# Optimization experiments

Hardware: AMD Instinct MI355X
Metric: run time of the kernel (lower is better)

Reference implementation:

```python
import jax, jax.numpy as jnp
import numpy as np

N = 8          # num_nodes (forced: stack with deconv output of leading dim 64 = 8*8)
T = 10         # out_dim == num_steps (Conv1d(out_dim, 1, ...) runs over the time axis)
H = 64         # hidden_dim (forced: ConvTranspose1d in_channels=64)
E = 2 * N      # edges come in fwd/rev pairs; E/2 must equal N for avg_pool squeeze
NODE_IN = 512  # gat1 in_dim = x_feat width (510) + CNN_1 output (2)
EDGE_IN = 128


def _conv1d(x, w, b, pad):
    # x: [B, Cin, L], w: [Cout, Cin, K]
    y = jax.lax.conv_general_dilated(x, w, (1,), [(pad, pad)],
                                     dimension_numbers=('NCH', 'OIH', 'NCH'))
    return y + b[None, :, None]


def _gat(x, src, dst, ea, W, a_s, a_d, We, a_e, bias, heads, ch, concat):
    # PyG GATConv with edge_dim and default add_self_loops=True (mean-fill edge_attr)
    n = x.shape[0]
    loop = jnp.arange(n)
    src = jnp.concatenate([src, loop])
    dst = jnp.concatenate([dst, loop])
    ea = jnp.concatenate([ea, jnp.broadcast_to(ea.mean(0), (n, ea.shape[1]))], 0)
    h = (x @ W).reshape(n, heads, ch)                 # [N,H,C]
    he = (ea @ We).reshape(-1, heads, ch)             # [E+N,H,C]
    alpha = (h * a_s).sum(-1)[src] + (h * a_d).sum(-1)[dst] + (he * a_e).sum(-1)
    alpha = jax.nn.leaky_relu(alpha, 0.2)             # [E+N,H]
    amax = jax.ops.segment_max(alpha, dst, num_segments=n)
    ex = jnp.exp(alpha - amax[dst])
    den = jax.ops.segment_sum(ex, dst, num_segments=n)
    w = ex / (den[dst] + 1e-16)                       # scatter-softmax over dst
    out = jax.ops.segment_sum(w[:, :, None] * h[src], dst, num_segments=n)
    out = out.reshape(n, heads * ch) if concat else out.mean(1)
    return out + bias


def _forward(x_feat, x_feat_tmp, edge_attr, c1w1, c1b1, c1w2, c1b2,
             g1_lin, g1_as, g1_ad, g1_le, g1_ae, g1_b,
             g2_lin, g2_as, g2_ad, g2_le, g2_ae, g2_b,
             mlp_w1, mlp_b1, mlp_w2, mlp_b2,
             d1w, d1b, d2w, d2b, d3w, d3b,
             c2w1, c2b1, c2w2, c2b2, c2l1w, c2l1b, c2l2w, c2l2b,
             edge_index):
    src, dst = edge_index[0], edge_index[1]
    # ---- CNN_1 on rows 1 and 5 of x_feat_tmp ----
    t = jnp.stack([x_feat_tmp[1], x_feat_tmp[5]], axis=1)    # [N,2,T]
    t = t.reshape(2, N, T)                                   # torch .view semantics
    t = jax.nn.relu(_conv1d(t, c1w1, c1b1, 1))               # [2,N,T]
    t = _conv1d(jnp.transpose(t, (0, 2, 1)), c1w2, c1b2, 1)  # [2,1,N]
    x_ = jax.nn.relu(t.reshape(N, 2))                        # torch .view semantics
    # ---- GAT stack ----
    x = jnp.concatenate([x_feat, x_], axis=1)                # [N,512]
    x = jax.nn.relu(_gat(x, src, dst, edge_attr, g1_lin, g1_as, g1_ad,
                         g1_le, g1_ae, g1_b, 4, H, True))    # [N,256]
    ea_new = jax.nn.relu(edge_attr @ mlp_w1 + mlp_b1) @ mlp_w2 + mlp_b2  # [E,64]
    x = jax.nn.relu(_gat(x, src, dst, ea_new, g2_lin, g2_as, g2_ad,
                         g2_le, g2_ae, g2_b, 1, H, False))   # [N,64]
    # ---- ConvTranspose1d on length-1 input == einsum; avg_pool2d over nodes/edges ----
    x_pool = (jnp.einsum('ni,iot->not', x, d1w) + d1b[None, :, None]).mean(0)          # [64,10]
    ef = (jnp.einsum('ni,iot->not', ea_new[::2], d2w) + d2b[None, :, None]).mean(0)    # [64,10]
    er = (jnp.einsum('ni,iot->not', ea_new[1::2], d3w) + d3b[None, :, None]).mean(0)   # [64,10]
    inf = x_feat_tmp.reshape(N * N, T)                       # [64,10]
    # ---- CNN_2 ----
    c = jnp.stack([x_pool, inf, ef, er], axis=1)             # [64,4,10]
    c = _conv1d(c, c2w1, c2b1, 0)                            # [64,32,8]
    c = c.reshape(N * N, 32, 4, 2).max(-1)                   # MaxPool1d(2) -> [64,32,4]
    c = _conv1d(c, c2w2, c2b2, 0)                            # [64,64,2]
    c = c.reshape(N * N, 128)                                # Flatten(1,2)
    c = jax.nn.relu((c @ c2l1w + c2l1b) @ c2l2w + c2l2b)     # [64,10]
    return c.reshape(N, N, T)


def setup_inputs():
    ks = iter(jax.random.split(jax.random.key(0), 48))
    def rn(shape, s=0.1):
        return jax.random.normal(next(ks), shape, dtype=jnp.float32) * s
    return dict(
        x_feat=rn((N, NODE_IN - 2), 1.0),
        x_feat_tmp=rn((N, N, T), 1.0),
        edge_attr=rn((E, EDGE_IN), 1.0),
        c1w1=rn((N, N, 3)), c1b1=rn((N,)),
        c1w2=rn((1, T, 3)), c1b2=rn((1,)),
        g1_lin=rn((NODE_IN, 4 * H)), g1_as=rn((4, H)), g1_ad=rn((4, H)),
        g1_le=rn((EDGE_IN, 4 * H)), g1_ae=rn((4, H)), g1_b=rn((4 * H,)),
        g2_lin=rn((4 * H, H)), g2_as=rn((1, H)), g2_ad=rn((1, H)),
        g2_le=rn((H, H)), g2_ae=rn((1, H)), g2_b=rn((H,)),
        mlp_w1=rn((EDGE_IN, H)), mlp_b1=rn((H,)),
        mlp_w2=rn((H, H)), mlp_b2=rn((H,)),
        d1w=rn((H, H, 10)), d1b=rn((H,)),
        d2w=rn((H, H, 10)), d2b=rn((H,)),
        d3w=rn((H, H, 10)), d3b=rn((H,)),
        c2w1=rn((32, 4, 3)), c2b1=rn((32,)),
        c2w2=rn((64, 32, 3)), c2b2=rn((64,)),
        c2l1w=rn((128, 256)), c2l1b=rn((256,)),
        c2l2w=rn((256, T)), c2l2b=rn((T,)),
        edge_index=jax.random.randint(next(ks), (2, E), 0, N, dtype=jnp.int32),
    )


def reference(x_feat, x_feat_tmp, edge_attr, c1w1, c1b1, c1w2, c1b2,
              g1_lin, g1_as, g1_ad, g1_le, g1_ae, g1_b,
              g2_lin, g2_as, g2_ad, g2_le, g2_ae, g2_b,
              mlp_w1, mlp_b1, mlp_w2, mlp_b2,
              d1w, d1b, d2w, d2b, d3w, d3b,
              c2w1, c2b1, c2w2, c2b2, c2l1w, c2l1b, c2l2w, c2l2b,
              edge_index):
    return _forward(x_feat, x_feat_tmp, edge_attr, c1w1, c1b1, c1w2, c1b2,
                    g1_lin, g1_as, g1_ad, g1_le, g1_ae, g1_b,
                    g2_lin, g2_as, g2_ad, g2_le, g2_ae, g2_b,
                    mlp_w1, mlp_b1, mlp_w2, mlp_b2,
                    d1w, d1b, d2w, d2b, d3w, d3b,
                    c2w1, c2b1, c2w2, c2b2, c2l1w, c2l1b, c2l2w, c2l2b,
                    edge_index)
```

## Files before the change

kernel.cpp:

```cpp
#include <hip/hip_runtime.h>
#include <math.h>

#define WS_HXPART 0
#define WS_SMALL  16384
#define WS_XCNN   16384
#define WS_SE1    16400
#define WS_SE2    16468
#define WS_WF     16488
#define WS_BF     17768
#define WS_VM     17778

#define F_H    0
#define F_X1   2048
#define F_H2P  4096
#define F_H2   6144
#define F_X2   6656
#define F_G1AS 7168
#define F_G1AD 7424
#define F_G1B  7680
#define F_GL0  7936
#define F_GL1  8192
#define F_G2AS 8448
#define F_G2AD 8512
#define F_G2B  8576
#define F_SS1  8704
#define F_SD1  8736
#define F_AL1  8768
#define F_WT1  8864
#define F_MX1  8960
#define F_DN1  8992
#define F_A1   9024
#define F_SS2  9280
#define F_SD2  9288
#define F_AL2  9296
#define F_WT2  9320
#define F_MX2  9344
#define F_DN2  9352
#define F_A2   9360
#define F_SA   0
#define F_SW2  7680
#define F_SML  13824
#define SM_XCNN 0
#define SM_SE1  16
#define SM_SE2  84
#define SM_WF   104
#define SM_BF   1384
#define SM_VM   1394
#define F_SW1  15424
#define F_CIN  15808
#define F_ESRC 15968
#define F_EDST 15992
#define F_SB1  16016
#define F_SB2  16048
#define F_SDB  16112

__global__ __launch_bounds__(256) void k1_pre(
    const float* __restrict__ xf,   const float* __restrict__ xft,
    const float* __restrict__ ea,
    const float* __restrict__ c1w1, const float* __restrict__ c1b1,
    const float* __restrict__ c1w2, const float* __restrict__ c1b2,
    const float* __restrict__ g1lin,const float* __restrict__ g1le,
    const float* __restrict__ g1ae,
    const float* __restrict__ mw1,  const float* __restrict__ mb1,
    const float* __restrict__ mw2,  const float* __restrict__ mb2,
    const float* __restrict__ g2le, const float* __restrict__ g2ae,
    const float* __restrict__ l1w,  const float* __restrict__ l1b,
    const float* __restrict__ l2w,  const float* __restrict__ l2b,
    float* __restrict__ ws)
{
    const int b = blockIdx.x, tid = threadIdx.x;
    if (b < 8) {
        __shared__ float sx[512];
        const int k0 = b * 64;
        const int klen = (b == 7) ? 62 : 64;
        for (int idx = tid; idx < 512; idx += 256) {
            int n = idx >> 6, kk = idx & 63;
            sx[n * 64 + kk] = (kk < klen) ? xf[n * 510 + k0 + kk] : 0.f;
        }
        __syncthreads();
        float acc[8];
        #pragma unroll
        for (int n = 0; n < 8; ++n) acc[n] = 0.f;
        for (int kk = 0; kk < 64; ++kk) {
            float w = g1lin[(k0 + kk) * 256 + tid];
            #pragma unroll
            for (int n = 0; n < 8; ++n) acc[n] += sx[n * 64 + kk] * w;
        }
        #pragma unroll
        for (int n = 0; n < 8; ++n) ws[WS_HXPART + (b * 8 + n) * 256 + tid] = acc[n];
    } else if (b == 8) {
        __shared__ float sea[2048 + 128];
        __shared__ float sae[256], q1[512];
        for (int idx = tid; idx < 2048; idx += 256) sea[idx] = ea[idx];
        sae[tid] = g1ae[tid];
        __syncthreads();
        if (tid < 128) {
            float m = 0.f;
            for (int e = 0; e < 16; ++e) m += sea[e * 128 + tid];
            sea[2048 + tid] = m * (1.f / 16.f);
        }
        __syncthreads();
        for (int o = tid; o < 512; o += 256) {
            int k = o >> 2, hd = o & 3;
            float acc = 0.f;
            for (int c = 0; c < 64; ++c) acc += g1le[k * 256 + hd * 64 + c] * sae[hd * 64 + c];
            q1[o] = acc;
        }
        __syncthreads();
        if (tid < 64) {
            int e = tid >> 2, hd = tid & 3;
            float acc = 0.f;
            for (int k = 0; k < 128; ++k) acc += sea[e * 128 + k] * q1[k * 4 + hd];
            ws[WS_SE1 + tid] = acc;
        } else if (tid < 68) {
            int hd = tid - 64;
            float acc = 0.f;
            for (int k = 0; k < 128; ++k) acc += sea[2048 + k] * q1[k * 4 + hd];
            ws[WS_SE1 + 64 + hd] = acc;
        }
    } else if (b == 9) {
        __shared__ float sea[2048];
        __shared__ float tmp[1024];
        __shared__ float ean[17 * 64];
        __shared__ float sq2a[64], sq2[64];
        for (int idx = tid; idx < 2048; idx += 256) sea[idx] = ea[idx];
        if (tid < 64) sq2a[tid] = g2ae[tid];
        __syncthreads();
        for (int o = tid; o < 1024; o += 256) {
            int e = o >> 6, c = o & 63;
            float acc = mb1[c];
            for (int k = 0; k < 128; ++k) acc += sea[e * 128 + k] * mw1[k * 64 + c];
            tmp[o] = fmaxf(acc, 0.f);
        }
        __syncthreads();
        for (int o = tid; o < 1024; o += 256) {
            int e = o >> 6, c = o & 63;
            float acc = mb2[c];
            for (int k = 0; k < 64; ++k) acc += tmp[e * 64 + k] * mw2[k * 64 + c];
            ean[o] = acc;
        }
        __syncthreads();
        if (tid < 64) {
            float m = 0.f;
            for (int e = 0; e < 16; ++e) m += ean[e * 64 + tid];
            ean[1024 + tid] = m * (1.f / 16.f);
        } else if (tid < 128) {
            int c = tid - 64;
            float m = 0.f;
            for (int e = 0; e < 16; e += 2) m += ean[e * 64 + c];
            ws[WS_VM + 64 + c] = m * 0.125f;
        } else if (tid < 192) {
            int c = tid - 128;
            float m = 0.f;
            for (int e = 1; e < 16; e += 2) m += ean[e * 64 + c];
            ws[WS_VM + 128 + c] = m * 0.125f;
        }
        __syncthreads();
        if (tid < 64) {
            float acc = 0.f;
            for (int c = 0; c < 64; ++c) acc += g2le[tid * 64 + c] * sq2a[c];
            sq2[tid] = acc;
        }
        __syncthreads();
        if (tid < 16) {
            float acc = 0.f;
            for (int k = 0; k < 64; ++k) acc += ean[tid * 64 + k] * sq2[k];
            ws[WS_SE2 + tid] = acc;
        } else if (tid == 16) {
            float acc = 0.f;
            for (int k = 0; k < 64; ++k) acc += ean[1024 + k] * sq2[k];
            ws[WS_SE2 + 16] = acc;
        }
    } else if (b == 10) {
        __shared__ float t2[160], y1[160], y2[16];
        if (tid < 160) {
            int b_ = tid / 80, ch = (tid % 80) / 10, tt = tid % 10;
            int srow = ((ch & 1) == 0) ? 1 : 5;
            int n = 4 * b_ + (ch >> 1);
            t2[tid] = xft[srow * 80 + n * 10 + tt];
        }
        __syncthreads();
        if (tid < 160) {
            int b_ = tid / 80, co = (tid % 80) / 10, tt = tid % 10;
            float acc = c1b1[co];
            for (int ci = 0; ci < 8; ++ci)
                for (int k = 0; k < 3; ++k) {
                    int p = tt + k - 1;
                    if (p >= 0 && p < 10) acc += t2[b_ * 80 + ci * 10 + p] * c1w1[co * 24 + ci * 3 + k];
                }
            y1[tid] = fmaxf(acc, 0.f);
        }
        __syncthreads();
        if (tid < 16) {
            int b_ = tid >> 3, p = tid & 7;
            float acc = c1b2[0];
            for (int i = 0; i < 10; ++i)
                for (int k = 0; k < 3; ++k) {
                    int q = p + k - 1;
                    if (q >= 0 && q < 8) acc += y1[b_ * 80 + q * 10 + i] * c1w2[i * 3 + k];
                }
            y2[tid] = acc;
        }
        __syncthreads();
        if (tid < 16) ws[WS_XCNN + tid] = fmaxf(y2[tid], 0.f);
    } else {
        __shared__ float sl2[2560];
        for (int idx = tid; idx < 2560; idx += 256) sl2[idx] = l2w[idx];
        __syncthreads();
        const int m0 = (b - 11) * 32;
        for (int o = tid; o < 320; o += 256) {
            int ml = o / 10, t = o % 10, m = m0 + ml;
            float acc = 0.f;
            for (int j = 0; j < 256; ++j) acc += l1w[m * 256 + j] * sl2[j * 10 + t];
            ws[WS_WF + m * 10 + t] = acc;
        }
        if (b == 11 && tid < 10) {
            float acc = l2b[tid];
            for (int j = 0; j < 256; ++j) acc += l1b[j] * sl2[j * 10 + tid];
            ws[WS_BF + tid] = acc;
        }
    }
}

__global__ __launch_bounds__(512) void k2_main(
    const float* __restrict__ xft,
    const float* __restrict__ g1lin,
    const float* __restrict__ g1as, const float* __restrict__ g1ad,
    const float* __restrict__ g1b,
    const float* __restrict__ g2lin,
    const float* __restrict__ g2as, const float* __restrict__ g2ad,
    const float* __restrict__ g2b,
    const int* __restrict__ eidx,
    const float* __restrict__ d1w, const float* __restrict__ d1b,
    const float* __restrict__ d2w, const float* __restrict__ d2b,
    const float* __restrict__ d3w, const float* __restrict__ d3b,
    const float* __restrict__ c2w1, const float* __restrict__ c2b1,
    const float* __restrict__ c2w2, const float* __restrict__ c2b2,
    const float* __restrict__ ws, float* __restrict__ out)
{
    __shared__ float sm[16128];
    const int tid = threadIdx.x;
    const int r0 = blockIdx.x * 4;
    int* esrc = (int*)sm + F_ESRC;
    int* edst = (int*)sm + F_EDST;

    float rA[15], rW[12];
    #pragma unroll
    for (int i = 0; i < 15; ++i) {
        int idx = tid + 512 * i;
        int t = idx % 10, rl = (idx / 10) & 3, ii = idx / 40;
        int tau = ii >> 6, iC = ii & 63;
        const float* dw = (tau == 0) ? d1w : (tau == 1) ? d2w : d3w;
        rA[i] = dw[iC * 640 + (r0 + rl) * 10 + t];
    }
    #pragma unroll
    for (int i = 0; i < 12; ++i) rW[i] = c2w2[tid + 512 * i];
    for (int idx = tid; idx < 1600; idx += 512) sm[F_SML + idx] = ws[WS_SMALL + idx];
    for (int idx = tid; idx < 384;  idx += 512) sm[F_SW1 + idx] = c2w1[idx];
    if (tid < 256) {
        sm[F_G1AS + tid] = g1as[tid];
        sm[F_G1AD + tid] = g1ad[tid];
        sm[F_G1B  + tid] = g1b[tid];
        sm[F_GL0  + tid] = g1lin[510 * 256 + tid];
        sm[F_GL1  + tid] = g1lin[511 * 256 + tid];
    } else {
        int j = tid - 256;
        if (j < 64)       { sm[F_G2AS + j] = g2as[j]; sm[F_G2AD + j] = g2ad[j]; sm[F_G2B + j] = g2b[j]; }
        else if (j < 88)  { int i = j - 64;  esrc[i] = (i < 16) ? eidx[i] : i - 16;
                                             edst[i] = (i < 16) ? eidx[16 + i] : i - 16; }
        else if (j < 128) { int i = j - 88;  int rl = i / 10, t = i % 10;
                            sm[F_CIN + rl * 40 + 10 + t] = xft[(r0 + rl) * 10 + t]; }
        else if (j < 160) sm[F_SB1 + j - 128] = c2b1[j - 128];
        else if (j < 224) sm[F_SB2 + j - 160] = c2b2[j - 160];
        else if (j < 236) { int i = j - 224, tau = i / 4, rl = i % 4;
                            const float* db = (tau == 0) ? d1b : (tau == 1) ? d2b : d3b;
                            sm[F_SDB + i] = db[r0 + rl]; }
    }
    __syncthreads();

    {
        const int j = tid & 255, half = tid >> 8;
        for (int nl = 0; nl < 4; ++nl) {
            int n = half * 4 + nl;
            float acc = 0.f;
            #pragma unroll
            for (int cb = 0; cb < 8; ++cb) acc += ws[WS_HXPART + (cb * 8 + n) * 256 + j];
            acc += sm[F_SML + SM_XCNN + n * 2] * sm[F_GL0 + j]
                 + sm[F_SML + SM_XCNN + n * 2 + 1] * sm[F_GL1 + j];
            sm[F_H + n * 256 + j] = acc;
        }
    }
    __syncthreads();
    {
        int p = tid >> 4, g = tid & 15, n = p >> 2, hd = p & 3;
        float aS = 0.f, aD = 0.f;
        #pragma unroll
        for (int cc = 0; cc < 4; ++cc) {
            int c = (((cc + p) & 3) << 4) + g;
            float hv = sm[F_H + n * 256 + hd * 64 + c];
            aS += hv * sm[F_G1AS + hd * 64 + c];
            aD += hv * sm[F_G1AD + hd * 64 + c];
        }
        #pragma unroll
        for (int m = 8; m >= 1; m >>= 1) { aS += __shfl_xor(aS, m); aD += __shfl_xor(aD, m); }
        if (g == 0) { sm[F_SS1 + p] = aS; sm[F_SD1 + p] = aD; }
    }
    __syncthreads();
    if (tid < 96) {
        int e = tid >> 2, hd = tid & 3;
        float se = (e < 16) ? sm[F_SML + SM_SE1 + tid] : sm[F_SML + SM_SE1 + 64 + hd];
        float s = sm[F_SS1 + esrc[e] * 4 + hd] + sm[F_SD1 + edst[e] * 4 + hd] + se;
        sm[F_AL1 + tid] = (s > 0.f) ? s : 0.2f * s;
    }
    __syncthreads();
    {
        int p = tid >> 4, g = tid & 15, n = p >> 2, hd = p & 3;
        float v1 = (edst[g] == n) ? sm[F_AL1 + g * 4 + hd] : -1e30f;
        float v2 = (g < 8 && edst[g + 16] == n) ? sm[F_AL1 + (g + 16) * 4 + hd] : -1e30f;
        float mx = fmaxf(v1, v2);
        #pragma unroll
        for (int m = 8; m >= 1; m >>= 1) mx = fmaxf(mx, __shfl_xor(mx, m));
        float ex = expf(v1 - mx) + ((g < 8) ? expf(v2 - mx) : 0.f);
        #pragma unroll
        for (int m = 8; m >= 1; m >>= 1) ex += __shfl_xor(ex, m);
        if (g == 0) { sm[F_MX1 + p] = mx; sm[F_DN1 + p] = ex; }
    }
    __syncthreads();
    if (tid < 96) {
        int e = tid >> 2, hd = tid & 3, d = edst[e];
        sm[F_WT1 + tid] = expf(sm[F_AL1 + tid] - sm[F_MX1 + d * 4 + hd]) / (sm[F_DN1 + d * 4 + hd] + 1e-16f);
    }
    __syncthreads();
    if (tid < 256) {
        int s = tid >> 5, n = (tid >> 2) & 7, hd = tid & 3;
        float acc = 0.f;
        #pragma unroll
        for (int e = 0; e < 24; ++e)
            acc += (edst[e] == n && esrc[e] == s) ? sm[F_WT1 + e * 4 + hd] : 0.f;
        sm[F_A1 + tid] = acc;
    }
    __syncthreads();
    {
        const int j = tid & 255, half = tid >> 8, hd = j >> 6;
        for (int nl = 0; nl < 4; ++nl) {
            int n = half * 4 + nl;
            float acc = 0.f;
            #pragma unroll
            for (int s = 0; s < 8; ++s)
                acc += sm[F_A1 + s * 32 + n * 4 + hd] * sm[F_H + s * 256 + j];
            sm[F_X1 + n * 256 + j] = fmaxf(acc + sm[F_G1B + j], 0.f);
        }
    }
    __syncthreads();
    {
        const int kc = tid >> 7, sub = (tid >> 6) & 1, c = tid & 63;
        float p0 = 0.f, p1 = 0.f, p2 = 0.f, p3 = 0.f;
        for (int kk = 0; kk < 64; ++kk) {
            int k = kc * 64 + kk;
            float g = g2lin[k * 64 + c];
            p0 += sm[F_X1 + (sub * 4 + 0) * 256 + k] * g;
            p1 += sm[F_X1 + (sub * 4 + 1) * 256 + k] * g;
            p2 += sm[F_X1 + (sub * 4 + 2) * 256 + k] * g;
            p3 += sm[F_X1 + (sub * 4 + 3) * 256 + k] * g;
        }
        sm[F_H2P + kc * 512 + (sub * 4 + 0) * 64 + c] = p0;
        sm[F_H2P + kc * 512 + (sub * 4 + 1) * 64 + c] = p1;
        sm[F_H2P + kc * 512 + (sub * 4 + 2) * 64 + c] = p2;
        sm[F_H2P + kc * 512 + (sub * 4 + 3) * 64 + c] = p3;
    }
    __syncthreads();
    sm[F_H2 + tid] = sm[F_H2P + tid] + sm[F_H2P + 512 + tid]
                   + sm[F_H2P + 1024 + tid] + sm[F_H2P + 1536 + tid];
    __syncthreads();
    {
        int n = tid >> 6, c = tid & 63;
        float hv = sm[F_H2 + n * 64 + c];
        float aS = hv * sm[F_G2AS + c], aD = hv * sm[F_G2AD + c];
        #pragma unroll
        for (int m = 32; m >= 1; m >>= 1) { aS += __shfl_xor(aS, m); aD += __shfl_xor(aD, m); }
        if (c == 0) { sm[F_SS2 + n] = aS; sm[F_SD2 + n] = aD; }
    }
    __syncthreads();
    if (tid < 24) {
        float se = (tid < 16) ? sm[F_SML + SM_SE2 + tid] : sm[F_SML + SM_SE2 + 16];
        float s = sm[F_SS2 + esrc[tid]] + sm[F_SD2 + edst[tid]] + se;
        sm[F_AL2 + tid] = (s > 0.f) ? s : 0.2f * s;
    }
    __syncthreads();
    if (tid < 256) {
        int n = tid >> 5, g = tid & 31;
        float v = (g < 24 && edst[g] == n) ? sm[F_AL2 + g] : -1e30f;
        float mx = v;
        #pragma unroll
        for (int m = 16; m >= 1; m >>= 1) mx = fmaxf(mx, __shfl_xor(mx, m));
        float ex = expf(v - mx);
        #pragma unroll
        for (int m = 16; m >= 1; m >>= 1) ex += __shfl_xor(ex, m);
        if (g == 0) { sm[F_MX2 + n] = mx; sm[F_DN2 + n] = ex; }
    }
    __syncthreads();
    if (tid < 24) {
        int d = edst[tid];
        sm[F_WT2 + tid] = expf(sm[F_AL2 + tid] - sm[F_MX2 + d]) / (sm[F_DN2 + d] + 1e-16f);
    }
    __syncthreads();
    if (tid < 64) {
        int n = tid >> 3, s = tid & 7;
        float acc = 0.f;
        #pragma unroll
        for (int e = 0; e < 24; ++e)
            acc += (edst[e] == n && esrc[e] == s) ? sm[F_WT2 + e] : 0.f;
        sm[F_A2 + tid] = acc;
    }
    __syncthreads();
    {
        int n = tid >> 6, c = tid & 63;
        float acc = 0.f;
        #pragma unroll
        for (int s = 0; s < 8; ++s) acc += sm[F_A2 + n * 8 + s] * sm[F_H2 + s * 64 + c];
        sm[F_X2 + n * 64 + c] = fmaxf(acc + sm[F_G2B + c], 0.f);
    }
    __syncthreads();
    if (tid < 64) {
        float m = 0.f;
        #pragma unroll
        for (int n = 0; n < 8; ++n) m += sm[F_X2 + n * 64 + tid];
        sm[F_SML + SM_VM + tid] = m * 0.125f;
    }
    __syncthreads();

    #pragma unroll
    for (int i = 0; i < 15; ++i) sm[F_SA + tid + 512 * i] = rA[i];
    #pragma unroll
    for (int i = 0; i < 12; ++i) sm[F_SW2 + tid + 512 * i] = rW[i];
    __syncthreads();
    if (tid < 120) {
        int t = tid % 10, tau = (tid / 10) % 3, rl = tid / 30;
        float acc = sm[F_SDB + tau * 4 + rl];
        for (int i = 0; i < 64; ++i)
            acc += sm[F_SML + SM_VM + tau * 64 + i] * sm[F_SA + ((tau * 64 + i) * 4 + rl) * 10 + t];
        int ch = (tau == 0) ? 0 : (tau + 1);
        sm[F_CIN + rl * 40 + ch * 10 + t] = acc;
    }
    __syncthreads();
    for (int o = tid; o < 1024; o += 512) {
        int rl = o >> 8, co = (o >> 3) & 31, p = o & 7;
        float acc = sm[F_SB1 + co];
        #pragma unroll
        for (int ci = 0; ci < 4; ++ci)
            #pragma unroll
            for (int k = 0; k < 3; ++k)
                acc += sm[F_CIN + rl * 40 + ci * 10 + p + k] * sm[F_SW1 + co * 12 + ci * 3 + k];
        sm[F_SA + o] = acc;
    }
    __syncthreads();
    {
        int rl = tid >> 7, co = (tid >> 2) & 31, q = tid & 3;
        sm[F_SA + 1024 + tid] = fmaxf(sm[F_SA + rl * 256 + co * 8 + 2 * q],
                                      sm[F_SA + rl * 256 + co * 8 + 2 * q + 1]);
    }
    __syncthreads();
    {
        int rl = tid >> 7, m = tid & 127, co2 = m >> 1, p = m & 1;
        float acc = sm[F_SB2 + co2];
        for (int ci = 0; ci < 32; ++ci)
            #pragma unroll
            for (int k = 0; k < 3; ++k)
                acc += sm[F_SA + 1024 + rl * 128 + ci * 4 + p + k] * sm[F_SW2 + co2 * 96 + ci * 3 + k];
        sm[F_SA + 1536 + tid] = acc;
    }
    __syncthreads();
    if (tid < 40) {
        int rl = tid / 10, t = tid % 10;
        float acc = sm[F_SML + SM_BF + t];
        for (int m = 0; m < 128; ++m)
            acc += sm[F_SA + 1536 + rl * 128 + m] * sm[F_SML + SM_WF + m * 10 + t];
        out[(r0 + rl) * 10 + t] = fmaxf(acc, 0.f);
    }
}

extern "C" void kernel_launch(void* const* d_in, const int* in_sizes, int n_in,
                              void* d_out, int out_size, void* d_ws, size_t ws_size,
                              hipStream_t stream)
{
    const float* xf    = (const float*)d_in[0];
    const float* xft   = (const float*)d_in[1];
    const float* ea    = (const float*)d_in[2];
    const float* c1w1  = (const float*)d_in[3];
    const float* c1b1  = (const float*)d_in[4];
    const float* c1w2  = (const float*)d_in[5];
    const float* c1b2  = (const float*)d_in[6];
    const float* g1lin = (const float*)d_in[7];
    const float* g1as  = (const float*)d_in[8];
    const float* g1ad  = (const float*)d_in[9];
    const float* g1le  = (const float*)d_in[10];
    const float* g1ae  = (const float*)d_in[11];
    const float* g1b   = (const float*)d_in[12];
    const float* g2lin = (const float*)d_in[13];
    const float* g2as  = (const float*)d_in[14];
    const float* g2ad  = (const float*)d_in[15];
    const float* g2le  = (const float*)d_in[16];
    const float* g2ae  = (const float*)d_in[17];
    const float* g2b   = (const float*)d_in[18];
    const float* mw1   = (const float*)d_in[19];
    const float* mb1   = (const float*)d_in[20];
    const float* mw2   = (const float*)d_in[21];
    const float* mb2   = (const float*)d_in[22];
    const float* d1w   = (const float*)d_in[23];
    const float* d1b   = (const float*)d_in[24];
    const float* d2w   = (const float*)d_in[25];
    const float* d2b   = (const float*)d_in[26];
    const float* d3w   = (const float*)d_in[27];
    const float* d3b   = (const float*)d_in[28];
    const float* c2w1  = (const float*)d_in[29];
    const float* c2b1  = (const float*)d_in[30];
    const float* c2w2  = (const float*)d_in[31];
    const float* c2b2  = (const float*)d_in[32];
    const float* l1w   = (const float*)d_in[33];
    const float* l1b   = (const float*)d_in[34];
    const float* l2w   = (const float*)d_in[35];
    const float* l2b   = (const float*)d_in[36];
    const int*   eidx  = (const int*)d_in[37];
    float* ws  = (float*)d_ws;
    float* out = (float*)d_out;

    hipLaunchKernelGGL(k1_pre, dim3(15), dim3(256), 0, stream,
        xf, xft, ea, c1w1, c1b1, c1w2, c1b2,
        g1lin, g1le, g1ae, mw1, mb1, mw2, mb2,
        g2le, g2ae, l1w, l1b, l2w, l2b, ws);
    hipLaunchKernelGGL(k2_main, dim3(16), dim3(512), 0, stream,
        xft, g1lin, g1as, g1ad, g1b,
        g2lin, g2as, g2ad, g2b, eidx,
        d1w, d1b, d2w, d2b, d3w, d3b,
        c2w1, c2b1, c2w2, c2b2, ws, out);
}
```

Measured before the change: 33.13 us.

## Restructure pre-kernel split and shorten main-kernel sync chain

The pre-kernel splits the x@W1 contraction into 4 k-chunks instead of 8 and stores the partials interleaved, so the main kernel reads them with one float4 load per node. The edge-embedding projection is split across two blocks. The main kernel prefetches those partials into registers, folds the leaky-relu alpha computations and the maxpool into their consumers to remove several barriers, and splits the deconv and final linear reductions across threads with shuffles. It also warms g2lin with dummy loads. The trade is more redundant recomputation and register pressure in exchange for fewer synchronization stages.

```diff
diff --git a/kernel.cpp b/kernel.cpp
--- a/kernel.cpp
+++ b/kernel.cpp
@@ -2,50 +2,43 @@
 #include <math.h>
 
 #define WS_HXPART 0
-#define WS_SMALL  16384
-#define WS_XCNN   16384
-#define WS_SE1    16400
-#define WS_SE2    16468
-#define WS_WF     16488
-#define WS_BF     17768
-#define WS_VM     17778
+#define WS_SMALL  8192
+#define SM_XCNN 0
+#define SM_SE1A 16
+#define SM_SE1B 84
+#define SM_SE2  152
+#define SM_WF   172
+#define SM_BF   1452
+#define SM_VME  1462
+#define SM_SIZE 1600
 
 #define F_H    0
 #define F_X1   2048
 #define F_H2P  4096
-#define F_H2   6144
-#define F_X2   6656
-#define F_G1AS 7168
-#define F_G1AD 7424
-#define F_G1B  7680
-#define F_GL0  7936
-#define F_GL1  8192
-#define F_G2AS 8448
-#define F_G2AD 8512
-#define F_G2B  8576
-#define F_SS1  8704
-#define F_SD1  8736
-#define F_AL1  8768
-#define F_WT1  8864
-#define F_MX1  8960
-#define F_DN1  8992
-#define F_A1   9024
-#define F_SS2  9280
-#define F_SD2  9288
-#define F_AL2  9296
-#define F_WT2  9320
-#define F_MX2  9344
-#define F_DN2  9352
-#define F_A2   9360
-#define F_SA   0
+#define F_GL0  6144
+#define F_GL1  6400
+#define F_G1AS 6656
+#define F_G1AD 6912
+#define F_G1B  7168
+#define F_SS1  7424
+#define F_SD1  7456
+#define F_MX1  7488
+#define F_DN1  7520
+#define F_WT1  7552
 #define F_SW2  7680
+#define F_A1   7680
+#define F_H2   7936
+#define F_X2   8448
+#define F_G2AS 8960
+#define F_G2AD 9024
+#define F_G2B  9088
+#define F_SS2  9152
+#define F_SD2  9160
+#define F_MX2  9168
+#define F_DN2  9176
+#define F_A2   9184
+#define F_WT2  9248
 #define F_SML  13824
-#define SM_XCNN 0
-#define SM_SE1  16
-#define SM_SE2  84
-#define SM_WF   104
-#define SM_BF   1384
-#define SM_VM   1394
 #define F_SW1  15424
 #define F_CIN  15808
 #define F_ESRC 15968
@@ -53,6 +46,8 @@
 #define F_SB1  16016
 #define F_SB2  16048
 #define F_SDB  16112
+#define F_VM0  16128
+#define SM_TOT 16192
 
 __global__ __launch_bounds__(256) void k1_pre(
     const float* __restrict__ xf,   const float* __restrict__ xft,
@@ -69,56 +64,60 @@
     float* __restrict__ ws)
 {
     const int b = blockIdx.x, tid = threadIdx.x;
-    if (b < 8) {
-        __shared__ float sx[512];
-        const int k0 = b * 64;
-        const int klen = (b == 7) ? 62 : 64;
-        for (int idx = tid; idx < 512; idx += 256) {
-            int n = idx >> 6, kk = idx & 63;
-            sx[n * 64 + kk] = (kk < klen) ? xf[n * 510 + k0 + kk] : 0.f;
+    if (b < 4) {
+        __shared__ float sx[1024];
+        const int k0 = b * 128;
+        const int klen = (b == 3) ? 126 : 128;
+        for (int idx = tid; idx < 1024; idx += 256) {
+            int n = idx >> 7, kk = idx & 127;
+            sx[n * 128 + kk] = (kk < klen) ? xf[n * 510 + k0 + kk] : 0.f;
         }
         __syncthreads();
         float acc[8];
         #pragma unroll
         for (int n = 0; n < 8; ++n) acc[n] = 0.f;
-        for (int kk = 0; kk < 64; ++kk) {
+        for (int kk = 0; kk < 128; ++kk) {
             float w = g1lin[(k0 + kk) * 256 + tid];
             #pragma unroll
-            for (int n = 0; n < 8; ++n) acc[n] += sx[n * 64 + kk] * w;
-        }
-        #pragma unroll
-        for (int n = 0; n < 8; ++n) ws[WS_HXPART + (b * 8 + n) * 256 + tid] = acc[n];
-    } else if (b == 8) {
-        __shared__ float sea[2048 + 128];
-        __shared__ float sae[256], q1[512];
-        for (int idx = tid; idx < 2048; idx += 256) sea[idx] = ea[idx];
+            for (int n = 0; n < 8; ++n) acc[n] += sx[n * 128 + kk] * w;
+        }
+        #pragma unroll
+        for (int n = 0; n < 8; ++n)
+            ws[WS_HXPART + ((n * 256 + tid) << 2) + b] = acc[n];
+    } else if (b < 6) {
+        __shared__ float seaC[1088];
+        __shared__ float sae[256], q1h[256];
+        const int kh = b - 4, k0 = kh * 64;
+        for (int idx = tid; idx < 1024; idx += 256) {
+            int e = idx >> 6, kk = idx & 63;
+            seaC[e * 64 + kk] = ea[e * 128 + k0 + kk];
+        }
         sae[tid] = g1ae[tid];
         __syncthreads();
-        if (tid < 128) {
+        if (tid < 64) {
             float m = 0.f;
-            for (int e = 0; e < 16; ++e) m += sea[e * 128 + tid];
-            sea[2048 + tid] = m * (1.f / 16.f);
-        }
-        __syncthreads();
-        for (int o = tid; o < 512; o += 256) {
-            int k = o >> 2, hd = o & 3;
-            float acc = 0.f;
-            for (int c = 0; c < 64; ++c) acc += g1le[k * 256 + hd * 64 + c] * sae[hd * 64 + c];
-            q1[o] = acc;
-        }
-        __syncthreads();
-        if (tid < 64) {
+            for (int e = 0; e < 16; ++e) m += seaC[e * 64 + tid];
+            seaC[1024 + tid] = m * (1.f / 16.f);
+        }
+        __syncthreads();
+        {
+            int kk = tid >> 2, hd = tid & 3;
+            float acc = 0.f;
+            for (int c = 0; c < 64; ++c)
+                acc += g1le[(k0 + kk) * 256 + hd * 64 + c] * sae[hd * 64 + c];
+            q1h[tid] = acc;
+        }
+        __syncthreads();
+        if (tid < 68) {
             int e = tid >> 2, hd = tid & 3;
-            float acc = 0.f;
-            for (int k = 0; k < 128; ++k) acc += sea[e * 128 + k] * q1[k * 4 + hd];
-            ws[WS_SE1 + tid] = acc;
-        } else if (tid < 68) {
-            int hd = tid - 64;
-            float acc = 0.f;
-            for (int k = 0; k < 128; ++k) acc += sea[2048 + k] * q1[k * 4 + hd];
-            ws[WS_SE1 + 64 + hd] = acc;
-        }
-    } else if (b == 9) {
+            int row = (tid < 64) ? e : 16;
+            if (tid >= 64) hd = tid - 64;
+            float acc = 0.f;
+            for (int kk = 0; kk < 64; ++kk) acc += seaC[row * 64 + kk] * q1h[kk * 4 + hd];
+            int dst = (tid < 64) ? tid : (64 + hd);
+            ws[WS_SMALL + ((kh == 0) ? SM_SE1A : SM_SE1B) + dst] = acc;
+        }
+    } else if (b == 6) {
         __shared__ float sea[2048];
         __shared__ float tmp[1024];
         __shared__ float ean[17 * 64];
@@ -148,12 +147,12 @@
             int c = tid - 64;
             float m = 0.f;
             for (int e = 0; e < 16; e += 2) m += ean[e * 64 + c];
-            ws[WS_VM + 64 + c] = m * 0.125f;
+            ws[WS_SMALL + SM_VME + c] = m * 0.125f;
         } else if (tid < 192) {
             int c = tid - 128;
             float m = 0.f;
             for (int e = 1; e < 16; e += 2) m += ean[e * 64 + c];
-            ws[WS_VM + 128 + c] = m * 0.125f;
+            ws[WS_SMALL + SM_VME + 64 + c] = m * 0.125f;
         }
         __syncthreads();
         if (tid < 64) {
@@ -165,13 +164,13 @@
         if (tid < 16) {
             float acc = 0.f;
             for (int k = 0; k < 64; ++k) acc += ean[tid * 64 + k] * sq2[k];
-            ws[WS_SE2 + tid] = acc;
+            ws[WS_SMALL + SM_SE2 + tid] = acc;
         } else if (tid == 16) {
             float acc = 0.f;
             for (int k = 0; k < 64; ++k) acc += ean[1024 + k] * sq2[k];
-            ws[WS_SE2 + 16] = acc;
-        }
-    } else if (b == 10) {
+            ws[WS_SMALL + SM_SE2 + 16] = acc;
+        }
+    } else if (b == 7) {
         __shared__ float t2[160], y1[160], y2[16];
         if (tid < 160) {
             int b_ = tid / 80, ch = (tid % 80) / 10, tt = tid % 10;
@@ -202,22 +201,22 @@
             y2[tid] = acc;
         }
         __syncthreads();
-        if (tid < 16) ws[WS_XCNN + tid] = fmaxf(y2[tid], 0.f);
+        if (tid < 16) ws[WS_SMALL + SM_XCNN + tid] = fmaxf(y2[tid], 0.f);
     } else {
         __shared__ float sl2[2560];
         for (int idx = tid; idx < 2560; idx += 256) sl2[idx] = l2w[idx];
         __syncthreads();
-        const int m0 = (b - 11) * 32;
+        const int m0 = (b - 8) * 32;
         for (int o = tid; o < 320; o += 256) {
             int ml = o / 10, t = o % 10, m = m0 + ml;
             float acc = 0.f;
             for (int j = 0; j < 256; ++j) acc += l1w[m * 256 + j] * sl2[j * 10 + t];
-            ws[WS_WF + m * 10 + t] = acc;
-        }
-        if (b == 11 && tid < 10) {
+            ws[WS_SMALL + SM_WF + m * 10 + t] = acc;
+        }
+        if (b == 8 && tid < 10) {
             float acc = l2b[tid];
             for (int j = 0; j < 256; ++j) acc += l1b[j] * sl2[j * 10 + tid];
-            ws[WS_BF + tid] = acc;
+            ws[WS_SMALL + SM_BF + tid] = acc;
         }
     }
 }
@@ -238,25 +237,19 @@
     const float* __restrict__ c2w2, const float* __restrict__ c2b2,
     const float* __restrict__ ws, float* __restrict__ out)
 {
-    __shared__ float sm[16128];
+    __shared__ float sm[SM_TOT];
     const int tid = threadIdx.x;
     const int r0 = blockIdx.x * 4;
     int* esrc = (int*)sm + F_ESRC;
     int* edst = (int*)sm + F_EDST;
 
-    float rA[15], rW[12];
+    const int jj = tid & 255, hf = tid >> 8;
+    float4 rH[4];
     #pragma unroll
-    for (int i = 0; i < 15; ++i) {
-        int idx = tid + 512 * i;
-        int t = idx % 10, rl = (idx / 10) & 3, ii = idx / 40;
-        int tau = ii >> 6, iC = ii & 63;
-        const float* dw = (tau == 0) ? d1w : (tau == 1) ? d2w : d3w;
-        rA[i] = dw[iC * 640 + (r0 + rl) * 10 + t];
-    }
-    #pragma unroll
-    for (int i = 0; i < 12; ++i) rW[i] = c2w2[tid + 512 * i];
-    for (int idx = tid; idx < 1600; idx += 512) sm[F_SML + idx] = ws[WS_SMALL + idx];
-    for (int idx = tid; idx < 384;  idx += 512) sm[F_SW1 + idx] = c2w1[idx];
+    for (int nl = 0; nl < 4; ++nl)
+        rH[nl] = *(const float4*)&ws[WS_HXPART + (((hf * 4 + nl) * 256 + jj) << 2)];
+    if (tid < 400)
+        *(float4*)&sm[F_SML + tid * 4] = *(const float4*)&ws[WS_SMALL + tid * 4];
     if (tid < 256) {
         sm[F_G1AS + tid] = g1as[tid];
         sm[F_G1AD + tid] = g1ad[tid];
@@ -276,19 +269,32 @@
                             const float* db = (tau == 0) ? d1b : (tau == 1) ? d2b : d3b;
                             sm[F_SDB + i] = db[r0 + rl]; }
     }
-    __syncthreads();
-
-    {
-        const int j = tid & 255, half = tid >> 8;
-        for (int nl = 0; nl < 4; ++nl) {
-            int n = half * 4 + nl;
-            float acc = 0.f;
-            #pragma unroll
-            for (int cb = 0; cb < 8; ++cb) acc += ws[WS_HXPART + (cb * 8 + n) * 256 + j];
-            acc += sm[F_SML + SM_XCNN + n * 2] * sm[F_GL0 + j]
-                 + sm[F_SML + SM_XCNN + n * 2 + 1] * sm[F_GL1 + j];
-            sm[F_H + n * 256 + j] = acc;
-        }
+    for (int idx = tid; idx < 384; idx += 512) sm[F_SW1 + idx] = c2w1[idx];
+    float rA[15], rW[12];
+    {
+        int ii = tid / 40, rem = tid - (tid / 40) * 40;
+        #pragma unroll
+        for (int i = 0; i < 15; ++i) {
+            const float* dw = (ii < 64) ? d1w : (ii < 128) ? d2w : d3w;
+            rA[i] = dw[(ii & 63) * 640 + r0 * 10 + rem];
+            ii += 12; rem += 32; if (rem >= 40) { rem -= 40; ++ii; }
+        }
+    }
+    #pragma unroll
+    for (int i = 0; i < 12; ++i) rW[i] = c2w2[tid + 512 * i];
+    {
+        float p0 = g2lin[tid * 32], p1 = g2lin[tid * 32 + 16];
+        asm volatile("" :: "v"(p0), "v"(p1));
+    }
+    __syncthreads();
+
+    #pragma unroll
+    for (int nl = 0; nl < 4; ++nl) {
+        int n = hf * 4 + nl;
+        float acc = ((rH[nl].x + rH[nl].y) + rH[nl].z) + rH[nl].w;
+        acc += sm[F_SML + SM_XCNN + n * 2] * sm[F_GL0 + jj]
+             + sm[F_SML + SM_XCNN + n * 2 + 1] * sm[F_GL1 + jj];
+        sm[F_H + n * 256 + jj] = acc;
     }
     __syncthreads();
     {
@@ -306,17 +312,15 @@
         if (g == 0) { sm[F_SS1 + p] = aS; sm[F_SD1 + p] = aD; }
     }
     __syncthreads();
-    if (tid < 96) {
-        int e = tid >> 2, hd = tid & 3;
-        float se = (e < 16) ? sm[F_SML + SM_SE1 + tid] : sm[F_SML + SM_SE1 + 64 + hd];
-        float s = sm[F_SS1 + esrc[e] * 4 + hd] + sm[F_SD1 + edst[e] * 4 + hd] + se;
-        sm[F_AL1 + tid] = (s > 0.f) ? s : 0.2f * s;
-    }
-    __syncthreads();
     {
         int p = tid >> 4, g = tid & 15, n = p >> 2, hd = p & 3;
-        float v1 = (edst[g] == n) ? sm[F_AL1 + g * 4 + hd] : -1e30f;
-        float v2 = (g < 8 && edst[g + 16] == n) ? sm[F_AL1 + (g + 16) * 4 + hd] : -1e30f;
+        #define AL1(e) ({ int _e = (e); \
+            float _se = (_e < 16) ? (sm[F_SML+SM_SE1A+_e*4+hd] + sm[F_SML+SM_SE1B+_e*4+hd]) \
+                                  : (sm[F_SML+SM_SE1A+64+hd]   + sm[F_SML+SM_SE1B+64+hd]); \
+            float _s = sm[F_SS1 + esrc[_e]*4+hd] + sm[F_SD1 + edst[_e]*4+hd] + _se; \
+            (_s > 0.f) ? _s : 0.2f * _s; })
+        float v1 = (edst[g] == n) ? AL1(g) : -1e30f;
+        float v2 = (g < 8 && edst[g + 16] == n) ? AL1(g + 16) : -1e30f;
         float mx = fmaxf(v1, v2);
         #pragma unroll
         for (int m = 8; m >= 1; m >>= 1) mx = fmaxf(mx, __shfl_xor(mx, m));
@@ -328,7 +332,9 @@
     __syncthreads();
     if (tid < 96) {
         int e = tid >> 2, hd = tid & 3, d = edst[e];
-        sm[F_WT1 + tid] = expf(sm[F_AL1 + tid] - sm[F_MX1 + d * 4 + hd]) / (sm[F_DN1 + d * 4 + hd] + 1e-16f);
+        float al = AL1(e);
+        sm[F_WT1 + tid] = expf(al - sm[F_MX1 + d * 4 + hd]) / (sm[F_DN1 + d * 4 + hd] + 1e-16f);
+        #undef AL1
     }
     __syncthreads();
     if (tid < 256) {
@@ -341,14 +347,15 @@
     }
     __syncthreads();
     {
-        const int j = tid & 255, half = tid >> 8, hd = j >> 6;
+        const int hd = jj >> 6;
+        #pragma unroll
         for (int nl = 0; nl < 4; ++nl) {
-            int n = half * 4 + nl;
+            int n = hf * 4 + nl;
             float acc = 0.f;
             #pragma unroll
             for (int s = 0; s < 8; ++s)
-                acc += sm[F_A1 + s * 32 + n * 4 + hd] * sm[F_H + s * 256 + j];
-            sm[F_X1 + n * 256 + j] = fmaxf(acc + sm[F_G1B + j], 0.f);
+                acc += sm[F_A1 + s * 32 + n * 4 + hd] * sm[F_H + s * 256 + jj];
+            sm[F_X1 + n * 256 + jj] = fmaxf(acc + sm[F_G1B + jj], 0.f);
         }
     }
     __syncthreads();
@@ -367,41 +374,44 @@
         sm[F_H2P + kc * 512 + (sub * 4 + 1) * 64 + c] = p1;
         sm[F_H2P + kc * 512 + (sub * 4 + 2) * 64 + c] = p2;
         sm[F_H2P + kc * 512 + (sub * 4 + 3) * 64 + c] = p3;
-    }
-    __syncthreads();
-    sm[F_H2 + tid] = sm[F_H2P + tid] + sm[F_H2P + 512 + tid]
-                   + sm[F_H2P + 1024 + tid] + sm[F_H2P + 1536 + tid];
+        #pragma unroll
+        for (int i = 4; i < 12; ++i) sm[F_SW2 + tid + 512 * i] = rW[i];
+    }
     __syncthreads();
     {
         int n = tid >> 6, c = tid & 63;
-        float hv = sm[F_H2 + n * 64 + c];
+        float hv = sm[F_H2P + n * 64 + c] + sm[F_H2P + 512 + n * 64 + c]
+                 + sm[F_H2P + 1024 + n * 64 + c] + sm[F_H2P + 1536 + n * 64 + c];
+        sm[F_H2 + n * 64 + c] = hv;
         float aS = hv * sm[F_G2AS + c], aD = hv * sm[F_G2AD + c];
         #pragma unroll
         for (int m = 32; m >= 1; m >>= 1) { aS += __shfl_xor(aS, m); aD += __shfl_xor(aD, m); }
         if (c == 0) { sm[F_SS2 + n] = aS; sm[F_SD2 + n] = aD; }
     }
     __syncthreads();
-    if (tid < 24) {
-        float se = (tid < 16) ? sm[F_SML + SM_SE2 + tid] : sm[F_SML + SM_SE2 + 16];
-        float s = sm[F_SS2 + esrc[tid]] + sm[F_SD2 + edst[tid]] + se;
-        sm[F_AL2 + tid] = (s > 0.f) ? s : 0.2f * s;
-    }
-    __syncthreads();
-    if (tid < 256) {
-        int n = tid >> 5, g = tid & 31;
-        float v = (g < 24 && edst[g] == n) ? sm[F_AL2 + g] : -1e30f;
-        float mx = v;
-        #pragma unroll
-        for (int m = 16; m >= 1; m >>= 1) mx = fmaxf(mx, __shfl_xor(mx, m));
-        float ex = expf(v - mx);
-        #pragma unroll
-        for (int m = 16; m >= 1; m >>= 1) ex += __shfl_xor(ex, m);
-        if (g == 0) { sm[F_MX2 + n] = mx; sm[F_DN2 + n] = ex; }
+    {
+        #define AL2(e) ({ int _e = (e); \
+            float _s = sm[F_SS2 + esrc[_e]] + sm[F_SD2 + edst[_e]] \
+                     + sm[F_SML + SM_SE2 + ((_e < 16) ? _e : 16)]; \
+            (_s > 0.f) ? _s : 0.2f * _s; })
+        if (tid < 256) {
+            int n = tid >> 5, g = tid & 31;
+            float v = (g < 24 && edst[g] == n) ? AL2(g) : -1e30f;
+            float mx = v;
+            #pragma unroll
+            for (int m = 16; m >= 1; m >>= 1) mx = fmaxf(mx, __shfl_xor(mx, m));
+            float ex = expf(v - mx);
+            #pragma unroll
+            for (int m = 16; m >= 1; m >>= 1) ex += __shfl_xor(ex, m);
+            if (g == 0) { sm[F_MX2 + n] = mx; sm[F_DN2 + n] = ex; }
+        }
     }
     __syncthreads();
     if (tid < 24) {
         int d = edst[tid];
-        sm[F_WT2 + tid] = expf(sm[F_AL2 + tid] - sm[F_MX2 + d]) / (sm[F_DN2 + d] + 1e-16f);
+        float al = AL2(tid);
+        sm[F_WT2 + tid] = expf(al - sm[F_MX2 + d]) / (sm[F_DN2 + d] + 1e-16f);
+        #undef AL2
     }
     __syncthreads();
     if (tid < 64) {
@@ -425,22 +435,30 @@
         float m = 0.f;
         #pragma unroll
         for (int n = 0; n < 8; ++n) m += sm[F_X2 + n * 64 + tid];
-        sm[F_SML + SM_VM + tid] = m * 0.125f;
+        sm[F_VM0 + tid] = m * 0.125f;
     }
     __syncthreads();
 
     #pragma unroll
-    for (int i = 0; i < 15; ++i) sm[F_SA + tid + 512 * i] = rA[i];
+    for (int i = 0; i < 15; ++i) sm[tid + 512 * i] = rA[i];
     #pragma unroll
-    for (int i = 0; i < 12; ++i) sm[F_SW2 + tid + 512 * i] = rW[i];
-    __syncthreads();
-    if (tid < 120) {
-        int t = tid % 10, tau = (tid / 10) % 3, rl = tid / 30;
-        float acc = sm[F_SDB + tau * 4 + rl];
-        for (int i = 0; i < 64; ++i)
-            acc += sm[F_SML + SM_VM + tau * 64 + i] * sm[F_SA + ((tau * 64 + i) * 4 + rl) * 10 + t];
-        int ch = (tau == 0) ? 0 : (tau + 1);
-        sm[F_CIN + rl * 40 + ch * 10 + t] = acc;
+    for (int i = 0; i < 4; ++i) sm[F_SW2 + tid + 512 * i] = rW[i];
+    __syncthreads();
+    if (tid < 480) {
+        int o = tid >> 2, q = tid & 3;
+        int t = o % 10, tau = (o / 10) % 3, rl = o / 30;
+        float acc = 0.f;
+        for (int i = q * 16; i < q * 16 + 16; ++i) {
+            float vm = (tau == 0) ? sm[F_VM0 + i]
+                     : (tau == 1) ? sm[F_SML + SM_VME + i]
+                                  : sm[F_SML + SM_VME + 64 + i];
+            acc += vm * sm[(tau * 64 + i) * 40 + rl * 10 + t];
+        }
+        acc += __shfl_xor(acc, 2); acc += __shfl_xor(acc, 1);
+        if (q == 0) {
+            int ch = (tau == 0) ? 0 : (tau + 1);
+            sm[F_CIN + rl * 40 + ch * 10 + t] = acc + sm[F_SDB + tau * 4 + rl];
+        }
     }
     __syncthreads();
     for (int o = tid; o < 1024; o += 512) {
@@ -451,13 +469,7 @@
             #pragma unroll
             for (int k = 0; k < 3; ++k)
                 acc += sm[F_CIN + rl * 40 + ci * 10 + p + k] * sm[F_SW1 + co * 12 + ci * 3 + k];
-        sm[F_SA + o] = acc;
-    }
-    __syncthreads();
-    {
-        int rl = tid >> 7, co = (tid >> 2) & 31, q = tid & 3;
-        sm[F_SA + 1024 + tid] = fmaxf(sm[F_SA + rl * 256 + co * 8 + 2 * q],
-                                      sm[F_SA + rl * 256 + co * 8 + 2 * q + 1]);
+        sm[4096 + o] = acc;
     }
     __syncthreads();
     {
@@ -465,17 +477,22 @@
         float acc = sm[F_SB2 + co2];
         for (int ci = 0; ci < 32; ++ci)
             #pragma unroll
-            for (int k = 0; k < 3; ++k)
-                acc += sm[F_SA + 1024 + rl * 128 + ci * 4 + p + k] * sm[F_SW2 + co2 * 96 + ci * 3 + k];
-        sm[F_SA + 1536 + tid] = acc;
-    }
-    __syncthreads();
-    if (tid < 40) {
-        int rl = tid / 10, t = tid % 10;
-        float acc = sm[F_SML + SM_BF + t];
-        for (int m = 0; m < 128; ++m)
-            acc += sm[F_SA + 1536 + rl * 128 + m] * sm[F_SML + SM_WF + m * 10 + t];
-        out[(r0 + rl) * 10 + t] = fmaxf(acc, 0.f);
+            for (int k = 0; k < 3; ++k) {
+                int u0 = 4096 + rl * 256 + ci * 8 + 2 * (p + k);
+                acc += fmaxf(sm[u0], sm[u0 + 1]) * sm[F_SW2 + co2 * 96 + ci * 3 + k];
+            }
+        sm[1024 + rl * 128 + m] = acc;
+    }
+    __syncthreads();
+    if (tid < 320) {
+        int o = tid >> 3, l = tid & 7;
+        int rl = o / 10, t = o % 10;
+        float acc = 0.f;
+        for (int m = l * 16; m < l * 16 + 16; ++m)
+            acc += sm[1024 + rl * 128 + m] * sm[F_SML + SM_WF + m * 10 + t];
+        acc += __shfl_xor(acc, 4); acc += __shfl_xor(acc, 2); acc += __shfl_xor(acc, 1);
+        if (l == 0)
+            out[(r0 + rl) * 10 + t] = fmaxf(acc + sm[F_SML + SM_BF + t], 0.f);
     }
 }
 
@@ -524,7 +541,7 @@
     float* ws  = (float*)d_ws;
     float* out = (float*)d_out;
 
-    hipLaunchKernelGGL(k1_pre, dim3(15), dim3(256), 0, stream,
+    hipLaunchKernelGGL(k1_pre, dim3(12), dim3(256), 0, stream,
         xf, xft, ea, c1w1, c1b1, c1w2, c1b2,
         g1lin, g1le, g1ae, mw1, mb1, mw2, mb2,
         g2le, g2ae, l1w, l1b, l2w, l2b, ws);
```

Result: no change. 33.46 us, median of 3 (+1.0%).
